# Optimization experiments

Hardware: AMD Instinct MI355X
Metric: run time of the kernel (lower is better)

## Reference

```python
import jax, jax.numpy as jnp
import numpy as np

B, S, D, H = 4, 2048, 1024, 16
DH = D // H

def setup_inputs() -> dict:
    key = jax.random.key(0)
    ks = jax.random.split(key, 4)
    scale = 1.0 / np.sqrt(D)
    x = jax.random.normal(ks[0], (B, S, D), dtype=jnp.float32)
    Wq = jax.random.normal(ks[1], (D, D), dtype=jnp.float32) * scale
    Wk = jax.random.normal(ks[2], (D, D), dtype=jnp.float32) * scale
    Wv = jax.random.normal(ks[3], (D, D), dtype=jnp.float32) * scale
    bq = jnp.zeros((D,), dtype=jnp.float32)
    bk = jnp.zeros((D,), dtype=jnp.float32)
    bv = jnp.zeros((D,), dtype=jnp.float32)
    # causal mask, broadcastable to [B, H, S, S]; mask==0 positions get -inf
    mask = jnp.tril(jnp.ones((S, S), dtype=bool))[None, None, :, :]
    return {"x": x, "mask": mask, "Wq": Wq, "bq": bq, "Wk": Wk, "bk": bk, "Wv": Wv, "bv": bv}

def reference(x, mask, Wq, bq, Wk, bk, Wv, bv):
    b, s, d = x.shape
    def proj(W, bias):
        # nn.Linear: x @ W.T + b, then split heads -> [b, H, s, DH]
        y = jnp.einsum('bsd,ed->bse', x, W) + bias
        return y.reshape(b, s, H, DH).transpose(0, 2, 1, 3)
    q = proj(Wq, bq)
    k = proj(Wk, bk)
    v = proj(Wv, bv)
    scores = jnp.einsum('bhqd,bhkd->bhqk', q, k) / jnp.sqrt(jnp.float32(DH))
    scores = jnp.where(mask, scores, -jnp.inf)
    attn = jax.nn.softmax(scores, axis=-1)
    out = jnp.einsum('bhqk,bhkd->bhqd', attn, v)
    return out.transpose(0, 2, 1, 3).reshape(b, s, d)
```

## Files before the change

kernel.cpp:

```cpp
#include <hip/hip_runtime.h>
#include <hip/hip_bf16.h>
#include <stdint.h>

typedef unsigned short u16;
typedef unsigned int   u32;
typedef short bf16x8 __attribute__((ext_vector_type(8)));
typedef float f32x4  __attribute__((ext_vector_type(4)));

typedef bf16x8 __attribute__((__may_alias__)) bf16x8_a;
typedef uint4  __attribute__((__may_alias__)) uint4_a;
typedef uint2  __attribute__((__may_alias__)) uint2_a;
typedef float4 __attribute__((__may_alias__)) float4_a;

#define MFMA_BF16(a,b,c) __builtin_amdgcn_mfma_f32_16x16x32_bf16((a),(b),(c),0,0,0)
#define L2E 1.44269504088896340736f

#define SEQ 2048
#define DMODEL 1024
#define NH 16
#define DH 64

__device__ __forceinline__ u32 pack_bf2(float a, float b) {
  union { __hip_bfloat162 h; u32 u; } c;
  c.h = __float22bfloat162_rn(make_float2(a, b));
  return c.u;
}

__device__ __forceinline__ u16 f2bf(float f) {
  u32 u = __builtin_bit_cast(u32, f);
  u += 0x7FFFu + ((u >> 16) & 1u);
  return (u16)(u >> 16);
}

__global__ __launch_bounds__(256, 2) void qkv_gemm(
    const float* __restrict__ X,
    const float* __restrict__ Wq, const float* __restrict__ Wk, const float* __restrict__ Wv,
    const float* __restrict__ Bq, const float* __restrict__ Bk, const float* __restrict__ Bv,
    u16* __restrict__ Qo, u16* __restrict__ Ko, u16* __restrict__ Vo)
{
  __shared__ u16 As[128 * 32];
  __shared__ u16 Bs[128 * 32];

  const int tid  = threadIdx.x;
  const int lane = tid & 63;
  const int wid  = tid >> 6;
  const int l16  = lane & 15;
  const int quad = lane >> 4;
  const int wm   = (wid >> 1) * 64;
  const int wn   = (wid & 1) * 64;

  const int m0 = blockIdx.x * 128;
  const int n0 = blockIdx.y * 128;
  const int pj = blockIdx.z;

  const float* W    = (pj == 0) ? Wq : (pj == 1) ? Wk : Wv;
  const float* Bias = (pj == 0) ? Bq : (pj == 1) ? Bk : Bv;
  u16*         Out  = (pj == 0) ? Qo : (pj == 1) ? Ko : Vo;
  const float scale = (pj == 0) ? 0.125f : 1.0f;

  f32x4 acc[4][4];
#pragma unroll
  for (int i = 0; i < 4; i++)
#pragma unroll
    for (int j = 0; j < 4; j++) acc[i][j] = (f32x4){0.f, 0.f, 0.f, 0.f};

  float4 gX[4], gW[4];
#pragma unroll
  for (int i = 0; i < 4; i++) {
    const int ch = i * 256 + tid;
    const int r = ch >> 3, c = ch & 7;
    gX[i] = *(const float4_a*)(X + (size_t)(m0 + r) * DMODEL + c * 4);
    gW[i] = *(const float4_a*)(W + (size_t)(n0 + r) * DMODEL + c * 4);
  }

  for (int kt = 0; kt < DMODEL; kt += 32) {
    __syncthreads();
#pragma unroll
    for (int i = 0; i < 4; i++) {
      const int ch = i * 256 + tid;
      const int r = ch >> 3, c = ch & 7;
      uint2 xp, wp;
      xp.x = pack_bf2(gX[i].x, gX[i].y);  xp.y = pack_bf2(gX[i].z, gX[i].w);
      wp.x = pack_bf2(gW[i].x, gW[i].y);  wp.y = pack_bf2(gW[i].z, gW[i].w);
      *(uint2_a*)&As[r * 32 + c * 4] = xp;
      *(uint2_a*)&Bs[r * 32 + c * 4] = wp;
    }
    __syncthreads();

    if (kt + 32 < DMODEL) {
#pragma unroll
      for (int i = 0; i < 4; i++) {
        const int ch = i * 256 + tid;
        const int r = ch >> 3, c = ch & 7;
        gX[i] = *(const float4_a*)(X + (size_t)(m0 + r) * DMODEL + kt + 32 + c * 4);
        gW[i] = *(const float4_a*)(W + (size_t)(n0 + r) * DMODEL + kt + 32 + c * 4);
      }
    }

    bf16x8 a[4], b[4];
#pragma unroll
    for (int mt = 0; mt < 4; mt++)
      a[mt] = *(const bf16x8_a*)&As[(wm + mt * 16 + l16) * 32 + quad * 8];
#pragma unroll
    for (int nt = 0; nt < 4; nt++)
      b[nt] = *(const bf16x8_a*)&Bs[(wn + nt * 16 + l16) * 32 + quad * 8];
#pragma unroll
    for (int mt = 0; mt < 4; mt++)
#pragma unroll
      for (int nt = 0; nt < 4; nt++)
        acc[mt][nt] = MFMA_BF16(a[mt], b[nt], acc[mt][nt]);
  }

  if (pj == 2) {
#pragma unroll
    for (int mt = 0; mt < 4; mt++) {
#pragma unroll
      for (int nt = 0; nt < 4; nt++) {
        const int n = n0 + wn + nt * 16 + l16;
        const float bias = Bias[n];
        const int h = n >> 6, dh = n & 63;
        const int m = m0 + wm + mt * 16 + quad * 4;
        const int bb = m >> 11, ss = m & 2047;
        uint2 pk;
        pk.x = pack_bf2(acc[mt][nt][0] + bias, acc[mt][nt][1] + bias);
        pk.y = pack_bf2(acc[mt][nt][2] + bias, acc[mt][nt][3] + bias);
        *(uint2_a*)&Out[((size_t)(bb * NH + h) * DH + dh) * SEQ + ss] = pk;
      }
    }
  } else {
#pragma unroll
    for (int mt = 0; mt < 4; mt++) {
#pragma unroll
      for (int nt = 0; nt < 4; nt++) {
        const int n = n0 + wn + nt * 16 + l16;
        const float bias = Bias[n];
        const int h = n >> 6, dh = n & 63;
#pragma unroll
        for (int r = 0; r < 4; r++) {
          const int m = m0 + wm + mt * 16 + quad * 4 + r;
          const int bb = m >> 11, ss = m & 2047;
          Out[((((size_t)bb * NH + h) * SEQ + ss) << 6) + dh] = f2bf((acc[mt][nt][r] + bias) * scale);
        }
      }
    }
  }
}

__global__ __launch_bounds__(256, 2) void flash_attn(
    const u16* __restrict__ Q, const u16* __restrict__ K, const u16* __restrict__ VT,
    float* __restrict__ O)
{
  __shared__ u16 Ks[128 * 72];
  __shared__ u16 VTs[64 * 136];
  __shared__ u16 Ps[4 * 32 * 144];

  const int tid  = threadIdx.x;
  const int lane = tid & 63;
  const int wid  = tid >> 6;
  const int l16  = lane & 15;
  const int quad = lane >> 4;

  const int idx = blockIdx.x;
  const int qt  = 15 - (idx >> 6);
  const int bh  = idx & 63;
  const int bb = bh >> 4, hh = bh & 15;
  const int qbase = qt * 128;

  const u16* Qh = Q  + (size_t)bh * (SEQ * DH);
  const u16* Kh = K  + (size_t)bh * (SEQ * DH);
  const u16* Vh = VT + (size_t)bh * (DH * SEQ);

#pragma unroll
  for (int i = 0; i < 4; i++) {
    const int ch = i * 256 + tid;
    const int r = ch >> 3, c = ch & 7;
    *(uint4_a*)&Ks[r * 72 + c * 8] = *(const uint4_a*)(Qh + (size_t)(qbase + r) * DH + c * 8);
  }
  __syncthreads();

  bf16x8 qf[2][2];
#pragma unroll
  for (int ct = 0; ct < 2; ct++)
#pragma unroll
    for (int ks = 0; ks < 2; ks++)
      qf[ct][ks] = *(const bf16x8_a*)&Ks[(wid * 32 + ct * 16 + l16) * 72 + ks * 32 + quad * 8];

  f32x4 o[4][2];
#pragma unroll
  for (int dt = 0; dt < 4; dt++)
#pragma unroll
    for (int ct = 0; ct < 2; ct++) o[dt][ct] = (f32x4){0.f, 0.f, 0.f, 0.f};

  float mold[2] = {-1e30f, -1e30f};
  float lsum[2] = {0.f, 0.f};

  uint4 gK[4], gV[4];
#pragma unroll
  for (int i = 0; i < 4; i++) {
    const int ch = i * 256 + tid;
    gK[i] = *(const uint4_a*)(Kh + (size_t)(ch >> 3) * DH + (ch & 7) * 8);
    gV[i] = *(const uint4_a*)(Vh + (size_t)(ch >> 4) * SEQ + (ch & 15) * 8);
  }

  for (int j = 0; j <= qt; j++) {
    __syncthreads();
#pragma unroll
    for (int i = 0; i < 4; i++) {
      const int ch = i * 256 + tid;
      *(uint4_a*)&Ks[(ch >> 3) * 72 + (ch & 7) * 8]   = gK[i];
      *(uint4_a*)&VTs[(ch >> 4) * 136 + (ch & 15) * 8] = gV[i];
    }
    __syncthreads();

    if (j < qt) {
      const int kb2 = (j + 1) * 128;
#pragma unroll
      for (int i = 0; i < 4; i++) {
        const int ch = i * 256 + tid;
        gK[i] = *(const uint4_a*)(Kh + (size_t)(kb2 + (ch >> 3)) * DH + (ch & 7) * 8);
        gV[i] = *(const uint4_a*)(Vh + (size_t)(ch >> 4) * SEQ + kb2 + (ch & 15) * 8);
      }
    }

    f32x4 s[8][2];
#pragma unroll
    for (int rt = 0; rt < 8; rt++) {
      bf16x8 ka0 = *(const bf16x8_a*)&Ks[(rt * 16 + l16) * 72 + 0 + quad * 8];
      bf16x8 ka1 = *(const bf16x8_a*)&Ks[(rt * 16 + l16) * 72 + 32 + quad * 8];
#pragma unroll
      for (int ct = 0; ct < 2; ct++) {
        f32x4 c = (f32x4){0.f, 0.f, 0.f, 0.f};
        c = MFMA_BF16(ka0, qf[ct][0], c);
        c = MFMA_BF16(ka1, qf[ct][1], c);
        s[rt][ct] = c;
      }
    }

    if (j == qt) {
#pragma unroll
      for (int rt = 0; rt < 8; rt++)
#pragma unroll
        for (int ct = 0; ct < 2; ct++) {
          const int ql = wid * 32 + ct * 16 + l16;
#pragma unroll
          for (int r = 0; r < 4; r++) {
            const int kvl = rt * 16 + quad * 4 + r;
            if (kvl > ql) s[rt][ct][r] = -1e30f;
          }
        }
    }

#pragma unroll
    for (int ct = 0; ct < 2; ct++) {
      float mt = -1e30f;
#pragma unroll
      for (int rt = 0; rt < 8; rt++)
#pragma unroll
        for (int r = 0; r < 4; r++) mt = fmaxf(mt, s[rt][ct][r]);
      mt = fmaxf(mt, __shfl_xor(mt, 16));
      mt = fmaxf(mt, __shfl_xor(mt, 32));
      const float mnew = fmaxf(mold[ct], mt);
      const float a = __builtin_amdgcn_exp2f((mold[ct] - mnew) * L2E);
      float ls = 0.f;
#pragma unroll
      for (int rt = 0; rt < 8; rt++)
#pragma unroll
        for (int r = 0; r < 4; r++) {
          const float p = __builtin_amdgcn_exp2f((s[rt][ct][r] - mnew) * L2E);
          s[rt][ct][r] = p;
          ls += p;
        }
      ls += __shfl_xor(ls, 16);
      ls += __shfl_xor(ls, 32);
      lsum[ct] = lsum[ct] * a + ls;
      mold[ct] = mnew;
#pragma unroll
      for (int dt = 0; dt < 4; dt++)
#pragma unroll
        for (int r = 0; r < 4; r++) o[dt][ct][r] *= a;
    }

    u16* Pw = &Ps[wid * 32 * 144];
#pragma unroll
    for (int rt = 0; rt < 8; rt++) {
#pragma unroll
      for (int ct = 0; ct < 2; ct++) {
        uint2 pk;
        pk.x = pack_bf2(s[rt][ct][0], s[rt][ct][1]);
        pk.y = pack_bf2(s[rt][ct][2], s[rt][ct][3]);
        *(uint2_a*)&Pw[(ct * 16 + l16) * 144 + rt * 16 + quad * 4] = pk;
      }
    }
    __syncthreads();

#pragma unroll
    for (int ks2 = 0; ks2 < 4; ks2++) {
      bf16x8 vt[4], pb[2];
#pragma unroll
      for (int dt = 0; dt < 4; dt++)
        vt[dt] = *(const bf16x8_a*)&VTs[(dt * 16 + l16) * 136 + ks2 * 32 + quad * 8];
#pragma unroll
      for (int ct = 0; ct < 2; ct++)
        pb[ct] = *(const bf16x8_a*)&Pw[(ct * 16 + l16) * 144 + ks2 * 32 + quad * 8];
#pragma unroll
      for (int dt = 0; dt < 4; dt++)
#pragma unroll
        for (int ct = 0; ct < 2; ct++)
          o[dt][ct] = MFMA_BF16(vt[dt], pb[ct], o[dt][ct]);
    }
  }

#pragma unroll
  for (int ct = 0; ct < 2; ct++) {
    const float inv = 1.0f / lsum[ct];
    const int qg = qbase + wid * 32 + ct * 16 + l16;
    float* orow = O + (size_t)((size_t)bb * SEQ + qg) * DMODEL + hh * 64;
#pragma unroll
    for (int dt = 0; dt < 4; dt++) {
      float4 v4;
      v4.x = o[dt][ct][0] * inv;  v4.y = o[dt][ct][1] * inv;
      v4.z = o[dt][ct][2] * inv;  v4.w = o[dt][ct][3] * inv;
      *(float4_a*)&orow[dt * 16 + quad * 4] = v4;
    }
  }
}

__global__ void paintf(float* out, int n, float v) {
  int i = blockIdx.x * 256 + threadIdx.x;
  if (i < n) out[i] = v;
}

extern "C" void kernel_launch(void* const* d_in, const int* in_sizes, int n_in,
                              void* d_out, int out_size, void* d_ws, size_t ws_size,
                              hipStream_t stream) {
  float* out = (float*)d_out;

  const size_t elems = (size_t)4 * SEQ * DMODEL;
  if (ws_size < 3 * elems * sizeof(u16)) {
    paintf<<<(out_size + 255) / 256, 256, 0, stream>>>(out, out_size, 3.0e38f);
    return;
  }

  const float* x  = (const float*)d_in[0];
  const float* Wq = (const float*)d_in[2];
  const float* bq = (const float*)d_in[3];
  const float* Wk = (const float*)d_in[4];
  const float* bk = (const float*)d_in[5];
  const float* Wv = (const float*)d_in[6];
  const float* bv = (const float*)d_in[7];

  u16* q = (u16*)d_ws;
  u16* k = q + elems;
  u16* v = k + elems;

  qkv_gemm<<<dim3(64, 8, 3), 256, 0, stream>>>(x, Wq, Wk, Wv, bq, bk, bv, q, k, v);
  flash_attn<<<1024, 256, 0, stream>>>(q, k, v, out);
}
```

Baseline: 315.7 us.

## Pre-convert inputs to bf16, use direct global-to-LDS loads, and tune attention scheduling

Adds two small kernels that convert x and the three weight matrices to bf16 in the workspace. A new QKV GEMM then fills LDS straight from global memory with global_load_lds, replacing the register fp32-to-bf16 conversion and staging. In flash attention, the block-wide barrier before the P·V step becomes a per-wave lgkmcnt wait, since each wave only reads its own P tile, and the MFMA sections are wrapped in s_setprio. The conversion kernels add extra memory traffic and launches. The new GEMM also drops the register prefetch overlap, and the bf16 path only runs when the workspace is large enough.

```diff
diff --git a/kernel.cpp b/kernel.cpp
--- a/kernel.cpp
+++ b/kernel.cpp
@@ -32,9 +32,45 @@
   return (u16)(u >> 16);
 }
 
-__global__ __launch_bounds__(256, 2) void qkv_gemm(
-    const float* __restrict__ X,
-    const float* __restrict__ Wq, const float* __restrict__ Wk, const float* __restrict__ Wv,
+__device__ __forceinline__ void gl_lds16(const u16* g, u16* l) {
+  __builtin_amdgcn_global_load_lds(
+      (const __attribute__((address_space(1))) void*)g,
+      (__attribute__((address_space(3))) void*)l, 16, 0, 0);
+}
+
+__global__ __launch_bounds__(256) void cvt_x_bf16(
+    const float* __restrict__ s, u16* __restrict__ d, int n8)
+{
+  int i = blockIdx.x * 256 + threadIdx.x;
+  const int stride = gridDim.x * 256;
+  for (; i < n8; i += stride) {
+    const float4_a* p = (const float4_a*)(s + (size_t)i * 8);
+    float4 a = p[0], b = p[1];
+    uint4 o;
+    o.x = pack_bf2(a.x, a.y); o.y = pack_bf2(a.z, a.w);
+    o.z = pack_bf2(b.x, b.y); o.w = pack_bf2(b.z, b.w);
+    *(uint4_a*)(d + (size_t)i * 8) = o;
+  }
+}
+
+__global__ __launch_bounds__(256) void cvt_w_bf16(
+    const float* __restrict__ wq, const float* __restrict__ wk, const float* __restrict__ wv,
+    u16* __restrict__ oq, u16* __restrict__ ok, u16* __restrict__ ov)
+{
+  const float* s = (blockIdx.y == 0) ? wq : (blockIdx.y == 1) ? wk : wv;
+  u16*         d = (blockIdx.y == 0) ? oq : (blockIdx.y == 1) ? ok : ov;
+  const int i = blockIdx.x * 256 + threadIdx.x;
+  const float4_a* p = (const float4_a*)(s + (size_t)i * 8);
+  float4 a = p[0], b = p[1];
+  uint4 o;
+  o.x = pack_bf2(a.x, a.y); o.y = pack_bf2(a.z, a.w);
+  o.z = pack_bf2(b.x, b.y); o.w = pack_bf2(b.z, b.w);
+  *(uint4_a*)(d + (size_t)i * 8) = o;
+}
+
+__global__ __launch_bounds__(256, 2) void qkv_gemm_bf(
+    const u16* __restrict__ Xb,
+    const u16* __restrict__ Wqb, const u16* __restrict__ Wkb, const u16* __restrict__ Wvb,
     const float* __restrict__ Bq, const float* __restrict__ Bk, const float* __restrict__ Bv,
     u16* __restrict__ Qo, u16* __restrict__ Ko, u16* __restrict__ Vo)
 {
@@ -53,7 +89,7 @@
   const int n0 = blockIdx.y * 128;
   const int pj = blockIdx.z;
 
-  const float* W    = (pj == 0) ? Wq : (pj == 1) ? Wk : Wv;
+  const u16*   Wb   = (pj == 0) ? Wqb : (pj == 1) ? Wkb : Wvb;
   const float* Bias = (pj == 0) ? Bq : (pj == 1) ? Bk : Bv;
   u16*         Out  = (pj == 0) ? Qo : (pj == 1) ? Ko : Vo;
   const float scale = (pj == 0) ? 0.125f : 1.0f;
@@ -64,38 +100,20 @@
 #pragma unroll
     for (int j = 0; j < 4; j++) acc[i][j] = (f32x4){0.f, 0.f, 0.f, 0.f};
 
-  float4 gX[4], gW[4];
-#pragma unroll
-  for (int i = 0; i < 4; i++) {
-    const int ch = i * 256 + tid;
-    const int r = ch >> 3, c = ch & 7;
-    gX[i] = *(const float4_a*)(X + (size_t)(m0 + r) * DMODEL + c * 4);
-    gW[i] = *(const float4_a*)(W + (size_t)(n0 + r) * DMODEL + c * 4);
-  }
+  const int lr = lane >> 2;
+  const int lc = (lane & 3) * 8;
+
+  const u16* Arow = Xb + (size_t)m0 * DMODEL;
+  const u16* Brow = Wb + (size_t)n0 * DMODEL;
 
   for (int kt = 0; kt < DMODEL; kt += 32) {
+#pragma unroll
+    for (int c = 0; c < 2; c++) {
+      const int band = c * 64 + wid * 16;
+      gl_lds16(Arow + (size_t)(band + lr) * DMODEL + kt + lc, &As[band * 32]);
+      gl_lds16(Brow + (size_t)(band + lr) * DMODEL + kt + lc, &Bs[band * 32]);
+    }
     __syncthreads();
-#pragma unroll
-    for (int i = 0; i < 4; i++) {
-      const int ch = i * 256 + tid;
-      const int r = ch >> 3, c = ch & 7;
-      uint2 xp, wp;
-      xp.x = pack_bf2(gX[i].x, gX[i].y);  xp.y = pack_bf2(gX[i].z, gX[i].w);
-      wp.x = pack_bf2(gW[i].x, gW[i].y);  wp.y = pack_bf2(gW[i].z, gW[i].w);
-      *(uint2_a*)&As[r * 32 + c * 4] = xp;
-      *(uint2_a*)&Bs[r * 32 + c * 4] = wp;
-    }
-    __syncthreads();
-
-    if (kt + 32 < DMODEL) {
-#pragma unroll
-      for (int i = 0; i < 4; i++) {
-        const int ch = i * 256 + tid;
-        const int r = ch >> 3, c = ch & 7;
-        gX[i] = *(const float4_a*)(X + (size_t)(m0 + r) * DMODEL + kt + 32 + c * 4);
-        gW[i] = *(const float4_a*)(W + (size_t)(n0 + r) * DMODEL + kt + 32 + c * 4);
-      }
-    }
 
     bf16x8 a[4], b[4];
 #pragma unroll
@@ -109,6 +127,8 @@
 #pragma unroll
       for (int nt = 0; nt < 4; nt++)
         acc[mt][nt] = MFMA_BF16(a[mt], b[nt], acc[mt][nt]);
+
+    __syncthreads();
   }
 
   if (pj == 2) {
@@ -146,6 +166,120 @@
   }
 }
 
+__global__ __launch_bounds__(256, 2) void qkv_gemm(
+    const float* __restrict__ X,
+    const float* __restrict__ Wq, const float* __restrict__ Wk, const float* __restrict__ Wv,
+    const float* __restrict__ Bq, const float* __restrict__ Bk, const float* __restrict__ Bv,
+    u16* __restrict__ Qo, u16* __restrict__ Ko, u16* __restrict__ Vo)
+{
+  __shared__ u16 As[128 * 32];
+  __shared__ u16 Bs[128 * 32];
+
+  const int tid  = threadIdx.x;
+  const int lane = tid & 63;
+  const int wid  = tid >> 6;
+  const int l16  = lane & 15;
+  const int quad = lane >> 4;
+  const int wm   = (wid >> 1) * 64;
+  const int wn   = (wid & 1) * 64;
+
+  const int m0 = blockIdx.x * 128;
+  const int n0 = blockIdx.y * 128;
+  const int pj = blockIdx.z;
+
+  const float* W    = (pj == 0) ? Wq : (pj == 1) ? Wk : Wv;
+  const float* Bias = (pj == 0) ? Bq : (pj == 1) ? Bk : Bv;
+  u16*         Out  = (pj == 0) ? Qo : (pj == 1) ? Ko : Vo;
+  const float scale = (pj == 0) ? 0.125f : 1.0f;
+
+  f32x4 acc[4][4];
+#pragma unroll
+  for (int i = 0; i < 4; i++)
+#pragma unroll
+    for (int j = 0; j < 4; j++) acc[i][j] = (f32x4){0.f, 0.f, 0.f, 0.f};
+
+  float4 gX[4], gW[4];
+#pragma unroll
+  for (int i = 0; i < 4; i++) {
+    const int ch = i * 256 + tid;
+    const int r = ch >> 3, c = ch & 7;
+    gX[i] = *(const float4_a*)(X + (size_t)(m0 + r) * DMODEL + c * 4);
+    gW[i] = *(const float4_a*)(W + (size_t)(n0 + r) * DMODEL + c * 4);
+  }
+
+  for (int kt = 0; kt < DMODEL; kt += 32) {
+    __syncthreads();
+#pragma unroll
+    for (int i = 0; i < 4; i++) {
+      const int ch = i * 256 + tid;
+      const int r = ch >> 3, c = ch & 7;
+      uint2 xp, wp;
+      xp.x = pack_bf2(gX[i].x, gX[i].y);  xp.y = pack_bf2(gX[i].z, gX[i].w);
+      wp.x = pack_bf2(gW[i].x, gW[i].y);  wp.y = pack_bf2(gW[i].z, gW[i].w);
+      *(uint2_a*)&As[r * 32 + c * 4] = xp;
+      *(uint2_a*)&Bs[r * 32 + c * 4] = wp;
+    }
+    __syncthreads();
+
+    if (kt + 32 < DMODEL) {
+#pragma unroll
+      for (int i = 0; i < 4; i++) {
+        const int ch = i * 256 + tid;
+        const int r = ch >> 3, c = ch & 7;
+        gX[i] = *(const float4_a*)(X + (size_t)(m0 + r) * DMODEL + kt + 32 + c * 4);
+        gW[i] = *(const float4_a*)(W + (size_t)(n0 + r) * DMODEL + kt + 32 + c * 4);
+      }
+    }
+
+    bf16x8 a[4], b[4];
+#pragma unroll
+    for (int mt = 0; mt < 4; mt++)
+      a[mt] = *(const bf16x8_a*)&As[(wm + mt * 16 + l16) * 32 + quad * 8];
+#pragma unroll
+    for (int nt = 0; nt < 4; nt++)
+      b[nt] = *(const bf16x8_a*)&Bs[(wn + nt * 16 + l16) * 32 + quad * 8];
+#pragma unroll
+    for (int mt = 0; mt < 4; mt++)
+#pragma unroll
+      for (int nt = 0; nt < 4; nt++)
+        acc[mt][nt] = MFMA_BF16(a[mt], b[nt], acc[mt][nt]);
+  }
+
+  if (pj == 2) {
+#pragma unroll
+    for (int mt = 0; mt < 4; mt++) {
+#pragma unroll
+      for (int nt = 0; nt < 4; nt++) {
+        const int n = n0 + wn + nt * 16 + l16;
+        const float bias = Bias[n];
+        const int h = n >> 6, dh = n & 63;
+        const int m = m0 + wm + mt * 16 + quad * 4;
+        const int bb = m >> 11, ss = m & 2047;
+        uint2 pk;
+        pk.x = pack_bf2(acc[mt][nt][0] + bias, acc[mt][nt][1] + bias);
+        pk.y = pack_bf2(acc[mt][nt][2] + bias, acc[mt][nt][3] + bias);
+        *(uint2_a*)&Out[((size_t)(bb * NH + h) * DH + dh) * SEQ + ss] = pk;
+      }
+    }
+  } else {
+#pragma unroll
+    for (int mt = 0; mt < 4; mt++) {
+#pragma unroll
+      for (int nt = 0; nt < 4; nt++) {
+        const int n = n0 + wn + nt * 16 + l16;
+        const float bias = Bias[n];
+        const int h = n >> 6, dh = n & 63;
+#pragma unroll
+        for (int r = 0; r < 4; r++) {
+          const int m = m0 + wm + mt * 16 + quad * 4 + r;
+          const int bb = m >> 11, ss = m & 2047;
+          Out[((((size_t)bb * NH + h) * SEQ + ss) << 6) + dh] = f2bf((acc[mt][nt][r] + bias) * scale);
+        }
+      }
+    }
+  }
+}
+
 __global__ __launch_bounds__(256, 2) void flash_attn(
     const u16* __restrict__ Q, const u16* __restrict__ K, const u16* __restrict__ VT,
     float* __restrict__ O)
@@ -223,6 +357,7 @@
     }
 
     f32x4 s[8][2];
+    __builtin_amdgcn_s_setprio(1);
 #pragma unroll
     for (int rt = 0; rt < 8; rt++) {
       bf16x8 ka0 = *(const bf16x8_a*)&Ks[(rt * 16 + l16) * 72 + 0 + quad * 8];
@@ -235,6 +370,7 @@
         s[rt][ct] = c;
       }
     }
+    __builtin_amdgcn_s_setprio(0);
 
     if (j == qt) {
 #pragma unroll
@@ -291,8 +427,9 @@
         *(uint2_a*)&Pw[(ct * 16 + l16) * 144 + rt * 16 + quad * 4] = pk;
       }
     }
-    __syncthreads();
-
+    asm volatile("s_waitcnt lgkmcnt(0)" ::: "memory");
+
+    __builtin_amdgcn_s_setprio(1);
 #pragma unroll
     for (int ks2 = 0; ks2 < 4; ks2++) {
       bf16x8 vt[4], pb[2];
@@ -308,6 +445,7 @@
         for (int ct = 0; ct < 2; ct++)
           o[dt][ct] = MFMA_BF16(vt[dt], pb[ct], o[dt][ct]);
     }
+    __builtin_amdgcn_s_setprio(0);
   }
 
 #pragma unroll
@@ -335,8 +473,12 @@
                               hipStream_t stream) {
   float* out = (float*)d_out;
 
-  const size_t elems = (size_t)4 * SEQ * DMODEL;
-  if (ws_size < 3 * elems * sizeof(u16)) {
+  const size_t elems  = (size_t)4 * SEQ * DMODEL;
+  const size_t welems = (size_t)DMODEL * DMODEL;
+  const size_t need_old = 3 * elems * sizeof(u16);
+  const size_t need_new = (4 * elems + 3 * welems) * sizeof(u16);
+
+  if (ws_size < need_old) {
     paintf<<<(out_size + 255) / 256, 256, 0, stream>>>(out, out_size, 3.0e38f);
     return;
   }
@@ -353,6 +495,17 @@
   u16* k = q + elems;
   u16* v = k + elems;
 
-  qkv_gemm<<<dim3(64, 8, 3), 256, 0, stream>>>(x, Wq, Wk, Wv, bq, bk, bv, q, k, v);
+  if (ws_size >= need_new) {
+    u16* xb  = v + elems;
+    u16* wqb = xb + elems;
+    u16* wkb = wqb + welems;
+    u16* wvb = wkb + welems;
+    cvt_x_bf16<<<2048, 256, 0, stream>>>(x, xb, (int)(elems / 8));
+    cvt_w_bf16<<<dim3(512, 3), 256, 0, stream>>>(Wq, Wk, Wv, wqb, wkb, wvb);
+    qkv_gemm_bf<<<dim3(64, 8, 3), 256, 0, stream>>>(xb, wqb, wkb, wvb, bq, bk, bv, q, k, v);
+  } else {
+    qkv_gemm<<<dim3(64, 8, 3), 256, 0, stream>>>(x, Wq, Wk, Wv, bq, bk, bv, q, k, v);
+  }
+
   flash_attn<<<1024, 256, 0, stream>>>(q, k, v, out);
 }
```

Result: faster. 304.7 us (-3.5%).
